# Kernel tuning notes

Hardware: AMD Instinct MI355X
Metric: run time of the kernel (lower is better)

The kernel has to match this reference:

```python
import jax, jax.numpy as jnp
import numpy as np


def _assoc_scan(gates, inputs, prev=None, remove_prev=None):
    """Linear recurrence out[t] = gates[t] * out[t-1] + inputs[t], scanned over axis 1.
    gates: (B, N, 1), inputs: (B, N, D), prev: (B, D) or None."""
    if remove_prev is None:
        remove_prev = prev is not None
    if prev is not None:
        inputs = jnp.concatenate([prev[:, None, :], inputs], axis=1)
        gates = jnp.concatenate([jnp.ones_like(gates[:, :1]), gates], axis=1)

    def combine(x, y):  # x earlier, y later
        xg, xv = x
        yg, yv = y
        return (yg * xg, yg * xv + yv)

    _, out = jax.lax.associative_scan(combine, (gates, inputs), axis=1)
    if remove_prev:
        out = out[:, 1:]
    return out


def setup_inputs() -> dict:
    key = jax.random.key(0)
    ks = jax.random.split(key, 7)
    B, N, D = 32, 2048, 512  # B = batch(4) * heads(8), D = flattened per-head param dim
    O = 2                    # momentum_order
    return {
        "W_t": jax.random.normal(ks[0], (B, D), jnp.float32),
        "x_t": jax.random.normal(ks[1], (4, N, 512), jnp.float32),  # unused by forward
        "grad_l_in": jax.random.normal(ks[2], (B, N, D), jnp.float32),
        "last_momentum": jax.random.normal(ks[3], (O, B, D), jnp.float32),
        "adaptive_momentum": jax.random.uniform(ks[4], (O, B, N, 1), dtype=jnp.float32),
        "combine_momentums": jax.random.uniform(ks[5], (O + 1, B, N), dtype=jnp.float32),
        "decay_factor": jax.random.uniform(ks[6], (B, N, 1), dtype=jnp.float32),
    }


def reference(W_t, x_t, grad_l_in, last_momentum, adaptive_momentum,
              combine_momentums, decay_factor):
    surprise = grad_l_in                       # (B, N, D)
    momentum = surprise
    momentums = []
    # sequential chain over momentum orders (small fixed count)
    for o in range(adaptive_momentum.shape[0]):
        momentum = _assoc_scan(adaptive_momentum[o], momentum, prev=last_momentum[o])
        momentums.append(momentum)
    momentums = jnp.stack(momentums)           # (O, B, N, D)
    next_last_momentum = momentums[:, :, -1]   # (O, B, D)
    # learned_combine_include_zeroth: prepend raw surprise as zeroth-order momentum
    momentums = jnp.concatenate([surprise[None], momentums], axis=0)  # (O+1, B, N, D)
    update = jnp.einsum('obn,obnd->bnd', combine_momentums, momentums)
    # final decay-weighted recurrence, keeping the prepended prev (remove_prev=False)
    update = _assoc_scan(1.0 - decay_factor, update, prev=W_t, remove_prev=False)  # (B, N+1, D)
    return update, next_last_momentum
```

## Files before the change

kernel.cpp:

```cpp
#include <hip/hip_runtime.h>

#define BB 32
#define NN 2048
#define DD 512
#define CC 32
#define LL (NN / CC)

typedef float vf2 __attribute__((ext_vector_type(2)));


__global__ __launch_bounds__(256) void pass1_local(
    const float* __restrict__ grad,
    const float* __restrict__ am,
    const float* __restrict__ cm,
    const float* __restrict__ dec,
    float* __restrict__ Mtot,
    float* __restrict__ local_end)
{
    const int c = blockIdx.x;
    const int b = blockIdx.y;
    const int d2 = threadIdx.x;
    const vf2* g2 = (const vf2*)grad;

    const float* a0p = am + (size_t)(0 * BB + b) * NN;
    const float* a1p = am + (size_t)(1 * BB + b) * NN;
    const float* c0p = cm + (size_t)(0 * BB + b) * NN;
    const float* c1p = cm + (size_t)(1 * BB + b) * NN;
    const float* c2p = cm + (size_t)(2 * BB + b) * NN;
    const float* dp  = dec + (size_t)b * NN;

    vf2 m0 = {0.f, 0.f}, m1 = {0.f, 0.f}, w = {0.f, 0.f};
    float p00 = 1.f, p10 = 0.f, p11 = 1.f, p20 = 0.f, p21 = 0.f, p22 = 1.f;

    const int t0 = c * LL;
    #pragma unroll 8
    for (int t = t0; t < t0 + LL; ++t) {
        const float a0 = a0p[t], a1 = a1p[t];
        const float c0 = c0p[t], c1 = c1p[t], c2 = c2p[t];
        const float e  = 1.0f - dp[t];
        const vf2 g = g2[(((size_t)(b * NN + t)) * DD >> 1) + d2];

        m0.x = fmaf(a0, m0.x, g.x);  m0.y = fmaf(a0, m0.y, g.y);
        m1.x = fmaf(a1, m1.x, m0.x); m1.y = fmaf(a1, m1.y, m0.y);
        w.x = fmaf(e, w.x, fmaf(c0, g.x, fmaf(c1, m0.x, c2 * m1.x)));
        w.y = fmaf(e, w.y, fmaf(c0, g.y, fmaf(c1, m0.y, c2 * m1.y)));

        const float k0 = (c1 + c2) * a0;
        const float k1 = c2 * a1;
        const float n00 = a0 * p00;
        const float n10 = fmaf(a0, p00, a1 * p10);
        const float n11 = a1 * p11;
        const float n20 = fmaf(k0, p00, fmaf(k1, p10, e * p20));
        const float n21 = fmaf(k1, p11, e * p21);
        const float n22 = e * p22;
        p00 = n00; p10 = n10; p11 = n11; p20 = n20; p21 = n21; p22 = n22;
    }

    vf2* le = (vf2*)local_end;
    const size_t base = ((size_t)(b * CC + c) * 3) * DD >> 1;
    le[base + d2]                 = m0;
    le[base + (DD >> 1) + d2]     = m1;
    le[base + 2 * (DD >> 1) + d2] = w;

    if (threadIdx.x == 0) {
        float* mt = Mtot + (size_t)(b * CC + c) * 6;
        mt[0] = p00; mt[1] = p10; mt[2] = p11;
        mt[3] = p20; mt[4] = p21; mt[5] = p22;
    }
}

__global__ __launch_bounds__(256) void pass3_fused(
    const float* __restrict__ grad,
    const float* __restrict__ am,
    const float* __restrict__ cm,
    const float* __restrict__ dec,
    const float* __restrict__ Wt,
    const float* __restrict__ lm,
    const float* __restrict__ Mtot,
    const float* __restrict__ local_end,
    float* __restrict__ out)
{
    const int c = blockIdx.x;
    const int b = blockIdx.y;
    const int d2 = threadIdx.x;

    const vf2* lm2 = (const vf2*)lm;
    const vf2* wt2 = (const vf2*)Wt;
    vf2 s0 = lm2[(((size_t)(0 * BB + b)) * DD >> 1) + d2];
    vf2 s1 = lm2[(((size_t)(1 * BB + b)) * DD >> 1) + d2];
    vf2 s2 = wt2[(((size_t)b) * DD >> 1) + d2];

    const vf2* le = (const vf2*)local_end;
    for (int cc = 0; cc < c; ++cc) {
        const float* mt = Mtot + (size_t)(b * CC + cc) * 6;
        const float p00 = mt[0], p10 = mt[1], p11 = mt[2];
        const float p20 = mt[3], p21 = mt[4], p22 = mt[5];

        const size_t base = ((size_t)(b * CC + cc) * 3) * DD >> 1;
        const vf2 l0 = le[base + d2];
        const vf2 l1 = le[base + (DD >> 1) + d2];
        const vf2 l2 = le[base + 2 * (DD >> 1) + d2];

        vf2 n0, n1, n2;
        n0.x = fmaf(p00, s0.x, l0.x);
        n0.y = fmaf(p00, s0.y, l0.y);
        n1.x = fmaf(p10, s0.x, fmaf(p11, s1.x, l1.x));
        n1.y = fmaf(p10, s0.y, fmaf(p11, s1.y, l1.y));
        n2.x = fmaf(p20, s0.x, fmaf(p21, s1.x, fmaf(p22, s2.x, l2.x)));
        n2.y = fmaf(p20, s0.y, fmaf(p21, s1.y, fmaf(p22, s2.y, l2.y)));
        s0 = n0; s1 = n1; s2 = n2;
    }

    vf2* out2 = (vf2*)out;
    if (c == 0) {
        __builtin_nontemporal_store(s2, &out2[(((size_t)b * (NN + 1)) * DD >> 1) + d2]);
    }

    const float* a0p = am + (size_t)(0 * BB + b) * NN;
    const float* a1p = am + (size_t)(1 * BB + b) * NN;
    const float* c0p = cm + (size_t)(0 * BB + b) * NN;
    const float* c1p = cm + (size_t)(1 * BB + b) * NN;
    const float* c2p = cm + (size_t)(2 * BB + b) * NN;
    const float* dp  = dec + (size_t)b * NN;

    const vf2* g2 = (const vf2*)grad;
    vf2 m0 = s0, m1 = s1, w = s2;

    const int t0 = c * LL;
    #pragma unroll 8
    for (int t = t0; t < t0 + LL; ++t) {
        const float a0 = a0p[t], a1 = a1p[t];
        const float c0 = c0p[t], c1 = c1p[t], c2 = c2p[t];
        const float e  = 1.0f - dp[t];
        const vf2 g = __builtin_nontemporal_load(
            &g2[(((size_t)(b * NN + t)) * DD >> 1) + d2]);

        m0.x = fmaf(a0, m0.x, g.x);  m0.y = fmaf(a0, m0.y, g.y);
        m1.x = fmaf(a1, m1.x, m0.x); m1.y = fmaf(a1, m1.y, m0.y);
        w.x = fmaf(e, w.x, fmaf(c0, g.x, fmaf(c1, m0.x, c2 * m1.x)));
        w.y = fmaf(e, w.y, fmaf(c0, g.y, fmaf(c1, m0.y, c2 * m1.y)));

        __builtin_nontemporal_store(
            w, &out2[(((size_t)(b * (NN + 1) + (t + 1))) * DD >> 1) + d2]);
    }

    if (c == CC - 1) {
        const size_t nlbase = ((size_t)BB * (NN + 1) * DD) >> 1;
        __builtin_nontemporal_store(
            m0, &out2[nlbase + (((size_t)(0 * BB + b)) * DD >> 1) + d2]);
        __builtin_nontemporal_store(
            m1, &out2[nlbase + (((size_t)(1 * BB + b)) * DD >> 1) + d2]);
    }
}

extern "C" void kernel_launch(void* const* d_in, const int* in_sizes, int n_in,
                              void* d_out, int out_size, void* d_ws, size_t ws_size,
                              hipStream_t stream) {
    const float* Wt   = (const float*)d_in[0];
    const float* grad = (const float*)d_in[2];
    const float* lm   = (const float*)d_in[3];
    const float* am   = (const float*)d_in[4];
    const float* cm   = (const float*)d_in[5];
    const float* dec  = (const float*)d_in[6];
    float* out = (float*)d_out;

    char* ws = (char*)d_ws;
    float* Mtot      = (float*)(ws);
    float* local_end = (float*)(ws + (size_t)BB * CC * 6 * sizeof(float));

    dim3 gridA(CC, BB);
    pass1_local<<<gridA, 256, 0, stream>>>(grad, am, cm, dec, Mtot, local_end);
    pass3_fused<<<gridA, 256, 0, stream>>>(grad, am, cm, dec, Wt, lm, Mtot,
                                           local_end, out);
}
```

Measured before the change: 83.54 us.

## Split scan into local write, serial carry pass, and carry-fixup pass

```diff
diff --git a/kernel.cpp b/kernel.cpp
--- a/kernel.cpp
+++ b/kernel.cpp
@@ -15,12 +15,14 @@
     const float* __restrict__ cm,
     const float* __restrict__ dec,
     float* __restrict__ Mtot,
-    float* __restrict__ local_end)
+    float* __restrict__ local_end,
+    float* __restrict__ out)
 {
     const int c = blockIdx.x;
     const int b = blockIdx.y;
     const int d2 = threadIdx.x;
     const vf2* g2 = (const vf2*)grad;
+    vf2* out2 = (vf2*)out;
 
     const float* a0p = am + (size_t)(0 * BB + b) * NN;
     const float* a1p = am + (size_t)(1 * BB + b) * NN;
@@ -38,12 +40,15 @@
         const float a0 = a0p[t], a1 = a1p[t];
         const float c0 = c0p[t], c1 = c1p[t], c2 = c2p[t];
         const float e  = 1.0f - dp[t];
-        const vf2 g = g2[(((size_t)(b * NN + t)) * DD >> 1) + d2];
+        const vf2 g = __builtin_nontemporal_load(
+            &g2[(((size_t)(b * NN + t)) * DD >> 1) + d2]);
 
         m0.x = fmaf(a0, m0.x, g.x);  m0.y = fmaf(a0, m0.y, g.y);
         m1.x = fmaf(a1, m1.x, m0.x); m1.y = fmaf(a1, m1.y, m0.y);
         w.x = fmaf(e, w.x, fmaf(c0, g.x, fmaf(c1, m0.x, c2 * m1.x)));
         w.y = fmaf(e, w.y, fmaf(c0, g.y, fmaf(c1, m0.y, c2 * m1.y)));
+
+        out2[(((size_t)(b * (NN + 1) + (t + 1))) * DD >> 1) + d2] = w;
 
         const float k0 = (c1 + c2) * a0;
         const float k1 = c2 * a1;
@@ -69,19 +74,15 @@
     }
 }
 
-__global__ __launch_bounds__(256) void pass3_fused(
-    const float* __restrict__ grad,
-    const float* __restrict__ am,
-    const float* __restrict__ cm,
-    const float* __restrict__ dec,
+__global__ __launch_bounds__(256) void pass2_carry(
     const float* __restrict__ Wt,
     const float* __restrict__ lm,
     const float* __restrict__ Mtot,
     const float* __restrict__ local_end,
+    float* __restrict__ carry,
     float* __restrict__ out)
 {
-    const int c = blockIdx.x;
-    const int b = blockIdx.y;
+    const int b = blockIdx.x;
     const int d2 = threadIdx.x;
 
     const vf2* lm2 = (const vf2*)lm;
@@ -90,13 +91,22 @@
     vf2 s1 = lm2[(((size_t)(1 * BB + b)) * DD >> 1) + d2];
     vf2 s2 = wt2[(((size_t)b) * DD >> 1) + d2];
 
+    vf2* out2 = (vf2*)out;
+    out2[(((size_t)b * (NN + 1)) * DD >> 1) + d2] = s2;
+
+    vf2* cy = (vf2*)carry;
     const vf2* le = (const vf2*)local_end;
-    for (int cc = 0; cc < c; ++cc) {
-        const float* mt = Mtot + (size_t)(b * CC + cc) * 6;
+
+    for (int c = 0; c < CC; ++c) {
+        const size_t base = ((size_t)(b * CC + c) * 3) * DD >> 1;
+        cy[base + d2]                 = s0;
+        cy[base + (DD >> 1) + d2]     = s1;
+        cy[base + 2 * (DD >> 1) + d2] = s2;
+
+        const float* mt = Mtot + (size_t)(b * CC + c) * 6;
         const float p00 = mt[0], p10 = mt[1], p11 = mt[2];
         const float p20 = mt[3], p21 = mt[4], p22 = mt[5];
 
-        const size_t base = ((size_t)(b * CC + cc) * 3) * DD >> 1;
         const vf2 l0 = le[base + d2];
         const vf2 l1 = le[base + (DD >> 1) + d2];
         const vf2 l2 = le[base + 2 * (DD >> 1) + d2];
@@ -111,10 +121,27 @@
         s0 = n0; s1 = n1; s2 = n2;
     }
 
-    vf2* out2 = (vf2*)out;
-    if (c == 0) {
-        __builtin_nontemporal_store(s2, &out2[(((size_t)b * (NN + 1)) * DD >> 1) + d2]);
-    }
+    const size_t nlbase = ((size_t)BB * (NN + 1) * DD) >> 1;
+    out2[nlbase + (((size_t)(0 * BB + b)) * DD >> 1) + d2] = s0;
+    out2[nlbase + (((size_t)(1 * BB + b)) * DD >> 1) + d2] = s1;
+}
+
+__global__ __launch_bounds__(256) void pass3_fix(
+    const float* __restrict__ am,
+    const float* __restrict__ cm,
+    const float* __restrict__ dec,
+    const float* __restrict__ carry,
+    float* __restrict__ out)
+{
+    const int c = blockIdx.x;
+    const int b = blockIdx.y;
+    const int d2 = threadIdx.x;
+
+    const vf2* cy = (const vf2*)carry;
+    const size_t base = ((size_t)(b * CC + c) * 3) * DD >> 1;
+    const vf2 s0 = cy[base + d2];
+    const vf2 s1 = cy[base + (DD >> 1) + d2];
+    const vf2 s2 = cy[base + 2 * (DD >> 1) + d2];
 
     const float* a0p = am + (size_t)(0 * BB + b) * NN;
     const float* a1p = am + (size_t)(1 * BB + b) * NN;
@@ -123,8 +150,8 @@
     const float* c2p = cm + (size_t)(2 * BB + b) * NN;
     const float* dp  = dec + (size_t)b * NN;
 
-    const vf2* g2 = (const vf2*)grad;
-    vf2 m0 = s0, m1 = s1, w = s2;
+    vf2* out2 = (vf2*)out;
+    float p00 = 1.f, p10 = 0.f, p11 = 1.f, p20 = 0.f, p21 = 0.f, p22 = 1.f;
 
     const int t0 = c * LL;
     #pragma unroll 8
@@ -132,24 +159,22 @@
         const float a0 = a0p[t], a1 = a1p[t];
         const float c0 = c0p[t], c1 = c1p[t], c2 = c2p[t];
         const float e  = 1.0f - dp[t];
-        const vf2 g = __builtin_nontemporal_load(
-            &g2[(((size_t)(b * NN + t)) * DD >> 1) + d2]);
-
-        m0.x = fmaf(a0, m0.x, g.x);  m0.y = fmaf(a0, m0.y, g.y);
-        m1.x = fmaf(a1, m1.x, m0.x); m1.y = fmaf(a1, m1.y, m0.y);
-        w.x = fmaf(e, w.x, fmaf(c0, g.x, fmaf(c1, m0.x, c2 * m1.x)));
-        w.y = fmaf(e, w.y, fmaf(c0, g.y, fmaf(c1, m0.y, c2 * m1.y)));
-
-        __builtin_nontemporal_store(
-            w, &out2[(((size_t)(b * (NN + 1) + (t + 1))) * DD >> 1) + d2]);
-    }
-
-    if (c == CC - 1) {
-        const size_t nlbase = ((size_t)BB * (NN + 1) * DD) >> 1;
-        __builtin_nontemporal_store(
-            m0, &out2[nlbase + (((size_t)(0 * BB + b)) * DD >> 1) + d2]);
-        __builtin_nontemporal_store(
-            m1, &out2[nlbase + (((size_t)(1 * BB + b)) * DD >> 1) + d2]);
+
+        const float k0 = (c1 + c2) * a0;
+        const float k1 = c2 * a1;
+        const float n00 = a0 * p00;
+        const float n10 = fmaf(a0, p00, a1 * p10);
+        const float n11 = a1 * p11;
+        const float n20 = fmaf(k0, p00, fmaf(k1, p10, e * p20));
+        const float n21 = fmaf(k1, p11, e * p21);
+        const float n22 = e * p22;
+        p00 = n00; p10 = n10; p11 = n11; p20 = n20; p21 = n21; p22 = n22;
+
+        const size_t idx = (((size_t)(b * (NN + 1) + (t + 1))) * DD >> 1) + d2;
+        vf2 wv = out2[idx];
+        wv.x = fmaf(p20, s0.x, fmaf(p21, s1.x, fmaf(p22, s2.x, wv.x)));
+        wv.y = fmaf(p20, s0.y, fmaf(p21, s1.y, fmaf(p22, s2.y, wv.y)));
+        out2[idx] = wv;
     }
 }
 
@@ -167,9 +192,11 @@
     char* ws = (char*)d_ws;
     float* Mtot      = (float*)(ws);
     float* local_end = (float*)(ws + (size_t)BB * CC * 6 * sizeof(float));
+    float* carry     = (float*)(ws + (size_t)BB * CC * 6 * sizeof(float)
+                                   + (size_t)BB * CC * 3 * DD * sizeof(float));
 
     dim3 gridA(CC, BB);
-    pass1_local<<<gridA, 256, 0, stream>>>(grad, am, cm, dec, Mtot, local_end);
-    pass3_fused<<<gridA, 256, 0, stream>>>(grad, am, cm, dec, Wt, lm, Mtot,
-                                           local_end, out);
-}
+    pass1_local<<<gridA, 256, 0, stream>>>(grad, am, cm, dec, Mtot, local_end, out);
+    pass2_carry<<<BB, 256, 0, stream>>>(Wt, lm, Mtot, local_end, carry, out);
+    pass3_fix<<<gridA, 256, 0, stream>>>(am, cm, dec, carry, out);
+}
```

Result: slower. 102.3 us (+22.5%).

## Split scan into two halves with separate carry-propagation kernel and vec4 loads

Applied to the files above, without the earlier changes.

```diff
diff --git a/kernel.cpp b/kernel.cpp
--- a/kernel.cpp
+++ b/kernel.cpp
@@ -3,24 +3,27 @@
 #define BB 32
 #define NN 2048
 #define DD 512
-#define CC 32
-#define LL (NN / CC)
-
-typedef float vf2 __attribute__((ext_vector_type(2)));
-
-
-__global__ __launch_bounds__(256) void pass1_local(
+#define CC 64
+#define LL 32
+#define HC 32
+#define D4 128
+
+typedef float vf4 __attribute__((ext_vector_type(4)));
+
+
+__global__ __launch_bounds__(128) void pass1_local(
     const float* __restrict__ grad,
     const float* __restrict__ am,
     const float* __restrict__ cm,
     const float* __restrict__ dec,
     float* __restrict__ Mtot,
-    float* __restrict__ local_end)
+    float* __restrict__ local_end,
+    int h)
 {
-    const int c = blockIdx.x;
+    const int c = blockIdx.x + h * HC;
     const int b = blockIdx.y;
-    const int d2 = threadIdx.x;
-    const vf2* g2 = (const vf2*)grad;
+    const int tid = threadIdx.x;
+    const vf4* g4 = (const vf4*)grad;
 
     const float* a0p = am + (size_t)(0 * BB + b) * NN;
     const float* a1p = am + (size_t)(1 * BB + b) * NN;
@@ -29,7 +32,7 @@
     const float* c2p = cm + (size_t)(2 * BB + b) * NN;
     const float* dp  = dec + (size_t)b * NN;
 
-    vf2 m0 = {0.f, 0.f}, m1 = {0.f, 0.f}, w = {0.f, 0.f};
+    vf4 m0 = {0.f, 0.f, 0.f, 0.f}, m1 = m0, w = m0;
     float p00 = 1.f, p10 = 0.f, p11 = 1.f, p20 = 0.f, p21 = 0.f, p22 = 1.f;
 
     const int t0 = c * LL;
@@ -38,12 +41,11 @@
         const float a0 = a0p[t], a1 = a1p[t];
         const float c0 = c0p[t], c1 = c1p[t], c2 = c2p[t];
         const float e  = 1.0f - dp[t];
-        const vf2 g = g2[(((size_t)(b * NN + t)) * DD >> 1) + d2];
-
-        m0.x = fmaf(a0, m0.x, g.x);  m0.y = fmaf(a0, m0.y, g.y);
-        m1.x = fmaf(a1, m1.x, m0.x); m1.y = fmaf(a1, m1.y, m0.y);
-        w.x = fmaf(e, w.x, fmaf(c0, g.x, fmaf(c1, m0.x, c2 * m1.x)));
-        w.y = fmaf(e, w.y, fmaf(c0, g.y, fmaf(c1, m0.y, c2 * m1.y)));
+        const vf4 g = g4[(size_t)(b * NN + t) * D4 + tid];
+
+        m0 = a0 * m0 + g;
+        m1 = a1 * m1 + m0;
+        w  = e * w + c0 * g + c1 * m0 + c2 * m1;
 
         const float k0 = (c1 + c2) * a0;
         const float k1 = c2 * a1;
@@ -56,65 +58,100 @@
         p00 = n00; p10 = n10; p11 = n11; p20 = n20; p21 = n21; p22 = n22;
     }
 
-    vf2* le = (vf2*)local_end;
-    const size_t base = ((size_t)(b * CC + c) * 3) * DD >> 1;
-    le[base + d2]                 = m0;
-    le[base + (DD >> 1) + d2]     = m1;
-    le[base + 2 * (DD >> 1) + d2] = w;
-
-    if (threadIdx.x == 0) {
+    vf4* le = (vf4*)local_end;
+    const size_t base = (size_t)(b * CC + c) * 3 * D4;
+    le[base + 0 * D4 + tid] = m0;
+    le[base + 1 * D4 + tid] = m1;
+    le[base + 2 * D4 + tid] = w;
+
+    if (tid == 0) {
         float* mt = Mtot + (size_t)(b * CC + c) * 6;
         mt[0] = p00; mt[1] = p10; mt[2] = p11;
         mt[3] = p20; mt[4] = p21; mt[5] = p22;
     }
 }
 
-__global__ __launch_bounds__(256) void pass3_fused(
+__global__ __launch_bounds__(128) void pass2_carry(
+    const float* __restrict__ Wt,
+    const float* __restrict__ lm,
+    const float* __restrict__ Mtot,
+    const float* __restrict__ local_end,
+    float* __restrict__ carry,
+    float* __restrict__ boundary,
+    float* __restrict__ out,
+    int h)
+{
+    const int b = blockIdx.x;
+    const int tid = threadIdx.x;
+
+    vf4 s0, s1, s2;
+    vf4* out4 = (vf4*)out;
+    vf4* bd = (vf4*)boundary;
+
+    if (h == 0) {
+        s0 = ((const vf4*)lm)[(size_t)(0 * BB + b) * D4 + tid];
+        s1 = ((const vf4*)lm)[(size_t)(1 * BB + b) * D4 + tid];
+        s2 = ((const vf4*)Wt)[(size_t)b * D4 + tid];
+        __builtin_nontemporal_store(s2, &out4[(size_t)(b * (NN + 1)) * D4 + tid]);
+    } else {
+        s0 = bd[(size_t)(0 * BB + b) * D4 + tid];
+        s1 = bd[(size_t)(1 * BB + b) * D4 + tid];
+        s2 = bd[(size_t)(2 * BB + b) * D4 + tid];
+    }
+
+    vf4* cy = (vf4*)carry;
+    const vf4* le = (const vf4*)local_end;
+
+    const int cbeg = h * HC;
+    for (int c = cbeg; c < cbeg + HC; ++c) {
+        const size_t base = (size_t)(b * CC + c) * 3 * D4;
+        cy[base + 0 * D4 + tid] = s0;
+        cy[base + 1 * D4 + tid] = s1;
+        cy[base + 2 * D4 + tid] = s2;
+
+        const float* mt = Mtot + (size_t)(b * CC + c) * 6;
+        const float p00 = mt[0], p10 = mt[1], p11 = mt[2];
+        const float p20 = mt[3], p21 = mt[4], p22 = mt[5];
+
+        const vf4 l0 = le[base + 0 * D4 + tid];
+        const vf4 l1 = le[base + 1 * D4 + tid];
+        const vf4 l2 = le[base + 2 * D4 + tid];
+
+        const vf4 n0 = p00 * s0 + l0;
+        const vf4 n1 = p10 * s0 + p11 * s1 + l1;
+        const vf4 n2 = p20 * s0 + p21 * s1 + p22 * s2 + l2;
+        s0 = n0; s1 = n1; s2 = n2;
+    }
+
+    if (h == 0) {
+        bd[(size_t)(0 * BB + b) * D4 + tid] = s0;
+        bd[(size_t)(1 * BB + b) * D4 + tid] = s1;
+        bd[(size_t)(2 * BB + b) * D4 + tid] = s2;
+    } else {
+        const size_t nl = (size_t)BB * (NN + 1) * D4;
+        __builtin_nontemporal_store(s0, &out4[nl + (size_t)(0 * BB + b) * D4 + tid]);
+        __builtin_nontemporal_store(s1, &out4[nl + (size_t)(1 * BB + b) * D4 + tid]);
+    }
+}
+
+__global__ __launch_bounds__(128) void pass3_final(
     const float* __restrict__ grad,
     const float* __restrict__ am,
     const float* __restrict__ cm,
     const float* __restrict__ dec,
-    const float* __restrict__ Wt,
-    const float* __restrict__ lm,
-    const float* __restrict__ Mtot,
-    const float* __restrict__ local_end,
-    float* __restrict__ out)
+    const float* __restrict__ carry,
+    float* __restrict__ out,
+    int h)
 {
-    const int c = blockIdx.x;
+    const int c = blockIdx.x + h * HC;
     const int b = blockIdx.y;
-    const int d2 = threadIdx.x;
-
-    const vf2* lm2 = (const vf2*)lm;
-    const vf2* wt2 = (const vf2*)Wt;
-    vf2 s0 = lm2[(((size_t)(0 * BB + b)) * DD >> 1) + d2];
-    vf2 s1 = lm2[(((size_t)(1 * BB + b)) * DD >> 1) + d2];
-    vf2 s2 = wt2[(((size_t)b) * DD >> 1) + d2];
-
-    const vf2* le = (const vf2*)local_end;
-    for (int cc = 0; cc < c; ++cc) {
-        const float* mt = Mtot + (size_t)(b * CC + cc) * 6;
-        const float p00 = mt[0], p10 = mt[1], p11 = mt[2];
-        const float p20 = mt[3], p21 = mt[4], p22 = mt[5];
-
-        const size_t base = ((size_t)(b * CC + cc) * 3) * DD >> 1;
-        const vf2 l0 = le[base + d2];
-        const vf2 l1 = le[base + (DD >> 1) + d2];
-        const vf2 l2 = le[base + 2 * (DD >> 1) + d2];
-
-        vf2 n0, n1, n2;
-        n0.x = fmaf(p00, s0.x, l0.x);
-        n0.y = fmaf(p00, s0.y, l0.y);
-        n1.x = fmaf(p10, s0.x, fmaf(p11, s1.x, l1.x));
-        n1.y = fmaf(p10, s0.y, fmaf(p11, s1.y, l1.y));
-        n2.x = fmaf(p20, s0.x, fmaf(p21, s1.x, fmaf(p22, s2.x, l2.x)));
-        n2.y = fmaf(p20, s0.y, fmaf(p21, s1.y, fmaf(p22, s2.y, l2.y)));
-        s0 = n0; s1 = n1; s2 = n2;
-    }
-
-    vf2* out2 = (vf2*)out;
-    if (c == 0) {
-        __builtin_nontemporal_store(s2, &out2[(((size_t)b * (NN + 1)) * DD >> 1) + d2]);
-    }
+    const int tid = threadIdx.x;
+
+    const vf4* cy = (const vf4*)carry;
+    const size_t base = (size_t)(b * CC + c) * 3 * D4;
+    vf4 m0 = cy[base + 0 * D4 + tid];
+    vf4 m1 = cy[base + 1 * D4 + tid];
+    vf4 w  = cy[base + 2 * D4 + tid];
 
     const float* a0p = am + (size_t)(0 * BB + b) * NN;
     const float* a1p = am + (size_t)(1 * BB + b) * NN;
@@ -123,8 +160,8 @@
     const float* c2p = cm + (size_t)(2 * BB + b) * NN;
     const float* dp  = dec + (size_t)b * NN;
 
-    const vf2* g2 = (const vf2*)grad;
-    vf2 m0 = s0, m1 = s1, w = s2;
+    const vf4* g4 = (const vf4*)grad;
+    vf4* out4 = (vf4*)out;
 
     const int t0 = c * LL;
     #pragma unroll 8
@@ -132,24 +169,14 @@
         const float a0 = a0p[t], a1 = a1p[t];
         const float c0 = c0p[t], c1 = c1p[t], c2 = c2p[t];
         const float e  = 1.0f - dp[t];
-        const vf2 g = __builtin_nontemporal_load(
-            &g2[(((size_t)(b * NN + t)) * DD >> 1) + d2]);
-
-        m0.x = fmaf(a0, m0.x, g.x);  m0.y = fmaf(a0, m0.y, g.y);
-        m1.x = fmaf(a1, m1.x, m0.x); m1.y = fmaf(a1, m1.y, m0.y);
-        w.x = fmaf(e, w.x, fmaf(c0, g.x, fmaf(c1, m0.x, c2 * m1.x)));
-        w.y = fmaf(e, w.y, fmaf(c0, g.y, fmaf(c1, m0.y, c2 * m1.y)));
+        const vf4 g = g4[(size_t)(b * NN + t) * D4 + tid];
+
+        m0 = a0 * m0 + g;
+        m1 = a1 * m1 + m0;
+        w  = e * w + c0 * g + c1 * m0 + c2 * m1;
 
         __builtin_nontemporal_store(
-            w, &out2[(((size_t)(b * (NN + 1) + (t + 1))) * DD >> 1) + d2]);
-    }
-
-    if (c == CC - 1) {
-        const size_t nlbase = ((size_t)BB * (NN + 1) * DD) >> 1;
-        __builtin_nontemporal_store(
-            m0, &out2[nlbase + (((size_t)(0 * BB + b)) * DD >> 1) + d2]);
-        __builtin_nontemporal_store(
-            m1, &out2[nlbase + (((size_t)(1 * BB + b)) * DD >> 1) + d2]);
+            w, &out4[(size_t)(b * (NN + 1) + t + 1) * D4 + tid]);
     }
 }
 
@@ -165,11 +192,16 @@
     float* out = (float*)d_out;
 
     char* ws = (char*)d_ws;
-    float* Mtot      = (float*)(ws);
+    float* Mtot      = (float*)ws;
     float* local_end = (float*)(ws + (size_t)BB * CC * 6 * sizeof(float));
-
-    dim3 gridA(CC, BB);
-    pass1_local<<<gridA, 256, 0, stream>>>(grad, am, cm, dec, Mtot, local_end);
-    pass3_fused<<<gridA, 256, 0, stream>>>(grad, am, cm, dec, Wt, lm, Mtot,
-                                           local_end, out);
-}
+    float* carry     = local_end + (size_t)BB * CC * 3 * DD;
+    float* boundary  = carry + (size_t)BB * CC * 3 * DD;
+
+    dim3 gridA(HC, BB);
+    for (int h = 0; h < 2; ++h) {
+        pass1_local<<<gridA, 128, 0, stream>>>(grad, am, cm, dec, Mtot, local_end, h);
+        pass2_carry<<<BB, 128, 0, stream>>>(Wt, lm, Mtot, local_end, carry,
+                                            boundary, out, h);
+        pass3_final<<<gridA, 128, 0, stream>>>(grad, am, cm, dec, carry, out, h);
+    }
+}
```

New measurement: 94.44 us. 13.0% more time.
